# Performance work log

Measured on AMD Instinct MI355X. Metric: run time of the kernel, lower is better.

Reference implementation:

```python
import jax, jax.numpy as jnp
import numpy as np

SEQ, BATCH, H = 512, 1024, 64  # hidden == input == 64 (8x8 grid)


def setup_inputs() -> dict:
    key = jax.random.key(0)
    k_x, k_wih, k_whh, k_bih, k_bhh = jax.random.split(key, 5)
    s = 1.0 / np.sqrt(H)  # PyTorch LSTM init scale U(-1/sqrt(H), 1/sqrt(H))
    x = jax.random.normal(k_x, (SEQ, BATCH, 8, 8), dtype=jnp.float32)
    W_ih = jax.random.uniform(k_wih, (4 * H, H), jnp.float32, -s, s)
    W_hh = jax.random.uniform(k_whh, (4 * H, H), jnp.float32, -s, s)
    b_ih = jax.random.uniform(k_bih, (4 * H,), jnp.float32, -s, s)
    b_hh = jax.random.uniform(k_bhh, (4 * H,), jnp.float32, -s, s)
    return {"x": x, "W_ih": W_ih, "W_hh": W_hh, "b_ih": b_ih, "b_hh": b_hh}


def _lstm(x_flat, W_ih, W_hh, b_ih, b_hh):
    # x_flat: (seq, batch, H). PyTorch gate order: i, f, g, o.
    seq, batch, _ = x_flat.shape
    # Precompute input projections for all timesteps in one big GEMM.
    xg = jnp.einsum('sbh,gh->sbg', x_flat, W_ih) + (b_ih + b_hh)  # (seq, batch, 4H)

    def step(carry, xg_t):
        h, c = carry
        gates = xg_t + h @ W_hh.T  # (batch, 4H)
        i, f, g, o = jnp.split(gates, 4, axis=-1)
        i = jax.nn.sigmoid(i)
        f = jax.nn.sigmoid(f)
        g = jnp.tanh(g)
        o = jax.nn.sigmoid(o)
        c = f * c + i * g
        h = o * jnp.tanh(c)
        return (h, c), h

    h0 = jnp.zeros((batch, W_hh.shape[1]), x_flat.dtype)
    c0 = jnp.zeros_like(h0)
    _, hs = jax.lax.scan(step, (h0, c0), xg)
    return hs  # (seq, batch, H)


def reference(x, W_ih, W_hh, b_ih, b_hh):
    seq, batch = x.shape[0], x.shape[1]
    x_flat = x.reshape(seq, batch, 64)  # Flatten(start_dim=2)
    hs = _lstm(x_flat, W_ih, W_hh, b_ih, b_hh)
    return hs.reshape(-1, 1024, 8, 8)
```

## Files before the change

kernel.cpp:

```cpp
#include <hip/hip_runtime.h>
#include <hip/hip_bf16.h>

#define SEQ   512
#define BATCH 1024
#define HD    64
#define NS    2
#define TB    16

typedef __attribute__((ext_vector_type(8))) short bf16x8;
typedef __attribute__((ext_vector_type(4))) float f32x4;

__device__ __forceinline__ unsigned short f2bf(float f) {
    unsigned u = __float_as_uint(f);
    return (unsigned short)((u + 0x7FFFu + ((u >> 16) & 1u)) >> 16);
}
__device__ __forceinline__ float frcp(float x) { return __builtin_amdgcn_rcpf(x); }
__device__ __forceinline__ float fsig(float x) { return frcp(1.f + __expf(-x)); }
__device__ __forceinline__ float ftanh(float x) { return 1.f - 2.f * frcp(__expf(2.f * x) + 1.f); }

__global__ __launch_bounds__(256, 2)
void lstm_v10(const float* __restrict__ x,
              const float* __restrict__ W_ih,
              const float* __restrict__ W_hh,
              const float* __restrict__ b_ih,
              const float* __restrict__ b_hh,
              float* __restrict__ out)
{
    __shared__ __align__(16) unsigned short xch[TB][NS][72];
    __shared__ __align__(16) float xg[NS][16][16][18];
    __shared__ __align__(16) unsigned short hb[2][NS][80];

    const int tid  = threadIdx.x;
    const int w    = tid >> 6;
    const int ln   = tid & 63;
    const int col  = ln & 15;
    const int kg   = ln >> 4;
    const int slot = (ln >> 2) & 1;
    const int q    = ln >> 4;
    const int qc   = q & 1;
    const int unit = w * 16 + col;
    const int sBase = blockIdx.x * NS;

    bf16x8 Bx[4][2], Bh[4][2];
    #pragma unroll
    for (int g = 0; g < 4; ++g) {
        #pragma unroll
        for (int kt = 0; kt < 2; ++kt) {
            const int n = (g * 4 + w) * 16 + col;
            const int k = kt * 32 + kg * 8;
            const float4 xa = *(const float4*)(W_ih + n * 64 + k);
            const float4 xb = *(const float4*)(W_ih + n * 64 + k + 4);
            const float4 ha = *(const float4*)(W_hh + n * 64 + k);
            const float4 hbq = *(const float4*)(W_hh + n * 64 + k + 4);
            bf16x8 vx, vh;
            vx[0]=(short)f2bf(xa.x); vx[1]=(short)f2bf(xa.y); vx[2]=(short)f2bf(xa.z); vx[3]=(short)f2bf(xa.w);
            vx[4]=(short)f2bf(xb.x); vx[5]=(short)f2bf(xb.y); vx[6]=(short)f2bf(xb.z); vx[7]=(short)f2bf(xb.w);
            vh[0]=(short)f2bf(ha.x); vh[1]=(short)f2bf(ha.y); vh[2]=(short)f2bf(ha.z); vh[3]=(short)f2bf(ha.w);
            vh[4]=(short)f2bf(hbq.x); vh[5]=(short)f2bf(hbq.y); vh[6]=(short)f2bf(hbq.z); vh[7]=(short)f2bf(hbq.w);
            Bx[g][kt] = vx; Bh[g][kt] = vh;
        }
    }
    float bs[4];
    #pragma unroll
    for (int g = 0; g < 4; ++g)
        bs[g] = b_ih[g * 64 + unit] + b_hh[g * 64 + unit];

    if (tid < 160) ((unsigned*)hb)[tid] = 0;

    float c_st = 0.f;
    int p = 0;
    const f32x4 z4 = {0.f, 0.f, 0.f, 0.f};
    float* outp = out + (size_t)(sBase + qc) * HD + unit;

    for (int T = 0; T < SEQ; T += TB) {
        #pragma unroll
        for (int j = 0; j < 2; ++j) {
            const int idx = tid + j * 256;
            const int k4 = idx & 15, sl = (idx >> 4) & 1, tt = idx >> 5;
            const float4 v = *(const float4*)&x[(((size_t)(T + tt) * BATCH) + sBase + sl) * HD + k4 * 4];
            uint2 pk;
            pk.x = (unsigned)f2bf(v.x) | ((unsigned)f2bf(v.y) << 16);
            pk.y = (unsigned)f2bf(v.z) | ((unsigned)f2bf(v.w) << 16);
            *(uint2*)&xch[tt][sl][k4 * 4] = pk;
        }
        __syncthreads();

        #pragma unroll
        for (int m = 0; m < NS; ++m) {
            const bf16x8 a0 = *(const bf16x8*)&xch[ln & 15][m][kg * 8];
            const bf16x8 a1 = *(const bf16x8*)&xch[ln & 15][m][32 + kg * 8];
            #pragma unroll
            for (int g = 0; g < 4; ++g) {
                f32x4 a = __builtin_amdgcn_mfma_f32_16x16x32_bf16(a0, Bx[g][0], z4, 0, 0, 0);
                a = __builtin_amdgcn_mfma_f32_16x16x32_bf16(a1, Bx[g][1], a, 0, 0, 0);
                *(f32x4*)&xg[m][g * 4 + w][col][4 * kg] = a;
            }
        }

        for (int tc = 0; tc < TB; ++tc) {
            const int t = T + tc;
            const float xgi = xg[qc][0 * 4 + w][col][tc];
            const float xgf = xg[qc][1 * 4 + w][col][tc];
            const float xgg = xg[qc][2 * 4 + w][col][tc];
            const float xgo = xg[qc][3 * 4 + w][col][tc];
            const bf16x8 ah0 = *(const bf16x8*)&hb[p][slot][kg * 8];
            const bf16x8 ah1 = *(const bf16x8*)&hb[p][slot][32 + kg * 8];

            __builtin_amdgcn_s_setprio(1);
            f32x4 a0 = __builtin_amdgcn_mfma_f32_16x16x32_bf16(ah0, Bh[0][0], z4, 0, 0, 0);
            f32x4 a1 = __builtin_amdgcn_mfma_f32_16x16x32_bf16(ah0, Bh[1][0], z4, 0, 0, 0);
            f32x4 a2 = __builtin_amdgcn_mfma_f32_16x16x32_bf16(ah0, Bh[2][0], z4, 0, 0, 0);
            f32x4 a3 = __builtin_amdgcn_mfma_f32_16x16x32_bf16(ah0, Bh[3][0], z4, 0, 0, 0);
            a0 = __builtin_amdgcn_mfma_f32_16x16x32_bf16(ah1, Bh[0][1], a0, 0, 0, 0);
            a1 = __builtin_amdgcn_mfma_f32_16x16x32_bf16(ah1, Bh[1][1], a1, 0, 0, 0);
            a2 = __builtin_amdgcn_mfma_f32_16x16x32_bf16(ah1, Bh[2][1], a2, 0, 0, 0);
            a3 = __builtin_amdgcn_mfma_f32_16x16x32_bf16(ah1, Bh[3][1], a3, 0, 0, 0);
            __builtin_amdgcn_s_setprio(0);

            if (ln < 32) {
                const float gi = xgi + a0[0] + bs[0];
                const float gf = xgf + a1[0] + bs[1];
                const float gg = xgg + a2[0] + bs[2];
                const float go = xgo + a3[0] + bs[3];
                const float iv = fsig(gi);
                const float fv = fsig(gf);
                const float gv = ftanh(gg);
                const float ov = fsig(go);
                c_st = fv * c_st + iv * gv;
                const float h  = ov * ftanh(c_st);
                outp[(size_t)t * (BATCH * HD)] = h;
                hb[p ^ 1][q][unit] = f2bf(h);
            }
            p ^= 1;
            __syncthreads();
        }
    }
}

extern "C" void kernel_launch(void* const* d_in, const int* in_sizes, int n_in,
                              void* d_out, int out_size, void* d_ws, size_t ws_size,
                              hipStream_t stream) {
    const float* x    = (const float*)d_in[0];
    const float* W_ih = (const float*)d_in[1];
    const float* W_hh = (const float*)d_in[2];
    const float* b_ih = (const float*)d_in[3];
    const float* b_hh = (const float*)d_in[4];
    float* out = (float*)d_out;

    lstm_v10<<<BATCH / NS, 256, 0, stream>>>(x, W_ih, W_hh, b_ih, b_hh, out);
}
```

Before: 191.1 us.

## Process four sequences per block and fold activation scaling into bf16 weights

Raises batch rows per block from 2 to 4 so all four MFMA row-quads do useful work, which halves the grid to 256 blocks at one block per CU. Pre-scales weights and bias by -log2(e) (or -2·log2(e) for the g gate) so activations become raw v_exp_f32 plus rcp, with tanh rewritten through sigmoid. Bias is folded into the MFMA accumulator init, the xg loads for the next step are issued early, the timestep loop is unrolled, and the MFMAs are split into independent K halves. Risks are lower occupancy with fewer blocks and extra bf16 rounding error from the scaled weights.

```diff
diff --git a/kernel.cpp b/kernel.cpp
--- a/kernel.cpp
+++ b/kernel.cpp
@@ -4,7 +4,7 @@
 #define SEQ   512
 #define BATCH 1024
 #define HD    64
-#define NS    2
+#define NS    4
 #define TB    16
 
 typedef __attribute__((ext_vector_type(8))) short bf16x8;
@@ -15,35 +15,39 @@
     return (unsigned short)((u + 0x7FFFu + ((u >> 16) & 1u)) >> 16);
 }
 __device__ __forceinline__ float frcp(float x) { return __builtin_amdgcn_rcpf(x); }
-__device__ __forceinline__ float fsig(float x) { return frcp(1.f + __expf(-x)); }
-__device__ __forceinline__ float ftanh(float x) { return 1.f - 2.f * frcp(__expf(2.f * x) + 1.f); }
+__device__ __forceinline__ float fexp2(float x) {
+    float r; asm("v_exp_f32 %0, %1" : "=v"(r) : "v"(x)); return r;
+}
 
-__global__ __launch_bounds__(256, 2)
-void lstm_v10(const float* __restrict__ x,
+__global__ __launch_bounds__(256, 1)
+void lstm_v11(const float* __restrict__ x,
               const float* __restrict__ W_ih,
               const float* __restrict__ W_hh,
               const float* __restrict__ b_ih,
               const float* __restrict__ b_hh,
               float* __restrict__ out)
 {
-    __shared__ __align__(16) unsigned short xch[TB][NS][72];
-    __shared__ __align__(16) float xg[NS][16][16][18];
-    __shared__ __align__(16) unsigned short hb[2][NS][80];
+    __shared__ __align__(16) float xg[NS][16][16][20];
+    __shared__ __align__(16) unsigned short xch[NS][TB][72];
+    __shared__ __align__(16) unsigned short hb[2][NS][88];
 
     const int tid  = threadIdx.x;
     const int w    = tid >> 6;
     const int ln   = tid & 63;
     const int col  = ln & 15;
     const int kg   = ln >> 4;
-    const int slot = (ln >> 2) & 1;
+    const int slot = (ln >> 2) & 3;
     const int q    = ln >> 4;
-    const int qc   = q & 1;
     const int unit = w * 16 + col;
     const int sBase = blockIdx.x * NS;
+
+    const float L2E = 1.4426950408889634f;
+    const float sc[4] = { -L2E, -L2E, -2.f * L2E, -L2E };
 
     bf16x8 Bx[4][2], Bh[4][2];
     #pragma unroll
     for (int g = 0; g < 4; ++g) {
+        const float s = sc[g];
         #pragma unroll
         for (int kt = 0; kt < 2; ++kt) {
             const int n = (g * 4 + w) * 16 + col;
@@ -51,87 +55,99 @@
             const float4 xa = *(const float4*)(W_ih + n * 64 + k);
             const float4 xb = *(const float4*)(W_ih + n * 64 + k + 4);
             const float4 ha = *(const float4*)(W_hh + n * 64 + k);
-            const float4 hbq = *(const float4*)(W_hh + n * 64 + k + 4);
+            const float4 hc = *(const float4*)(W_hh + n * 64 + k + 4);
             bf16x8 vx, vh;
-            vx[0]=(short)f2bf(xa.x); vx[1]=(short)f2bf(xa.y); vx[2]=(short)f2bf(xa.z); vx[3]=(short)f2bf(xa.w);
-            vx[4]=(short)f2bf(xb.x); vx[5]=(short)f2bf(xb.y); vx[6]=(short)f2bf(xb.z); vx[7]=(short)f2bf(xb.w);
-            vh[0]=(short)f2bf(ha.x); vh[1]=(short)f2bf(ha.y); vh[2]=(short)f2bf(ha.z); vh[3]=(short)f2bf(ha.w);
-            vh[4]=(short)f2bf(hbq.x); vh[5]=(short)f2bf(hbq.y); vh[6]=(short)f2bf(hbq.z); vh[7]=(short)f2bf(hbq.w);
+            vx[0]=(short)f2bf(xa.x*s); vx[1]=(short)f2bf(xa.y*s); vx[2]=(short)f2bf(xa.z*s); vx[3]=(short)f2bf(xa.w*s);
+            vx[4]=(short)f2bf(xb.x*s); vx[5]=(short)f2bf(xb.y*s); vx[6]=(short)f2bf(xb.z*s); vx[7]=(short)f2bf(xb.w*s);
+            vh[0]=(short)f2bf(ha.x*s); vh[1]=(short)f2bf(ha.y*s); vh[2]=(short)f2bf(ha.z*s); vh[3]=(short)f2bf(ha.w*s);
+            vh[4]=(short)f2bf(hc.x*s); vh[5]=(short)f2bf(hc.y*s); vh[6]=(short)f2bf(hc.z*s); vh[7]=(short)f2bf(hc.w*s);
             Bx[g][kt] = vx; Bh[g][kt] = vh;
         }
     }
-    float bs[4];
+    f32x4 bias4[4];
     #pragma unroll
-    for (int g = 0; g < 4; ++g)
-        bs[g] = b_ih[g * 64 + unit] + b_hh[g * 64 + unit];
+    for (int g = 0; g < 4; ++g) {
+        const int gg = g * 64 + unit;
+        const float b = (b_ih[gg] + b_hh[gg]) * sc[g];
+        bias4[g][0] = b; bias4[g][1] = b; bias4[g][2] = b; bias4[g][3] = b;
+    }
 
-    if (tid < 160) ((unsigned*)hb)[tid] = 0;
+    for (int i = tid; i < (2 * NS * 88) / 2; i += 256) ((unsigned*)hb)[i] = 0;
 
     float c_st = 0.f;
-    int p = 0;
     const f32x4 z4 = {0.f, 0.f, 0.f, 0.f};
-    float* outp = out + (size_t)(sBase + qc) * HD + unit;
+    float* outp = out + (size_t)(sBase + q) * HD + unit;
 
     for (int T = 0; T < SEQ; T += TB) {
         #pragma unroll
-        for (int j = 0; j < 2; ++j) {
+        for (int j = 0; j < 4; ++j) {
             const int idx = tid + j * 256;
-            const int k4 = idx & 15, sl = (idx >> 4) & 1, tt = idx >> 5;
-            const float4 v = *(const float4*)&x[(((size_t)(T + tt) * BATCH) + sBase + sl) * HD + k4 * 4];
+            const int k4 = idx & 15, tt = (idx >> 4) & 15, m = idx >> 8;
+            const float4 v = *(const float4*)&x[(((size_t)(T + tt) * BATCH) + sBase + m) * HD + k4 * 4];
             uint2 pk;
             pk.x = (unsigned)f2bf(v.x) | ((unsigned)f2bf(v.y) << 16);
             pk.y = (unsigned)f2bf(v.z) | ((unsigned)f2bf(v.w) << 16);
-            *(uint2*)&xch[tt][sl][k4 * 4] = pk;
+            *(uint2*)&xch[m][tt][k4 * 4] = pk;
         }
         __syncthreads();
 
         #pragma unroll
         for (int m = 0; m < NS; ++m) {
-            const bf16x8 a0 = *(const bf16x8*)&xch[ln & 15][m][kg * 8];
-            const bf16x8 a1 = *(const bf16x8*)&xch[ln & 15][m][32 + kg * 8];
+            const bf16x8 a0 = *(const bf16x8*)&xch[m][ln & 15][kg * 8];
+            const bf16x8 a1 = *(const bf16x8*)&xch[m][ln & 15][32 + kg * 8];
             #pragma unroll
             for (int g = 0; g < 4; ++g) {
-                f32x4 a = __builtin_amdgcn_mfma_f32_16x16x32_bf16(a0, Bx[g][0], z4, 0, 0, 0);
+                f32x4 a = __builtin_amdgcn_mfma_f32_16x16x32_bf16(a0, Bx[g][0], bias4[g], 0, 0, 0);
                 a = __builtin_amdgcn_mfma_f32_16x16x32_bf16(a1, Bx[g][1], a, 0, 0, 0);
                 *(f32x4*)&xg[m][g * 4 + w][col][4 * kg] = a;
             }
         }
 
+        float xgi = xg[q][0 * 4 + w][col][0];
+        float xgf = xg[q][1 * 4 + w][col][0];
+        float xgg = xg[q][2 * 4 + w][col][0];
+        float xgo = xg[q][3 * 4 + w][col][0];
+
+        #pragma unroll
         for (int tc = 0; tc < TB; ++tc) {
-            const int t = T + tc;
-            const float xgi = xg[qc][0 * 4 + w][col][tc];
-            const float xgf = xg[qc][1 * 4 + w][col][tc];
-            const float xgg = xg[qc][2 * 4 + w][col][tc];
-            const float xgo = xg[qc][3 * 4 + w][col][tc];
-            const bf16x8 ah0 = *(const bf16x8*)&hb[p][slot][kg * 8];
-            const bf16x8 ah1 = *(const bf16x8*)&hb[p][slot][32 + kg * 8];
+            const int pr = tc & 1;
+            const bf16x8 ah0 = *(const bf16x8*)&hb[pr][slot][kg * 8];
+            const bf16x8 ah1 = *(const bf16x8*)&hb[pr][slot][32 + kg * 8];
 
-            __builtin_amdgcn_s_setprio(1);
-            f32x4 a0 = __builtin_amdgcn_mfma_f32_16x16x32_bf16(ah0, Bh[0][0], z4, 0, 0, 0);
-            f32x4 a1 = __builtin_amdgcn_mfma_f32_16x16x32_bf16(ah0, Bh[1][0], z4, 0, 0, 0);
-            f32x4 a2 = __builtin_amdgcn_mfma_f32_16x16x32_bf16(ah0, Bh[2][0], z4, 0, 0, 0);
-            f32x4 a3 = __builtin_amdgcn_mfma_f32_16x16x32_bf16(ah0, Bh[3][0], z4, 0, 0, 0);
-            a0 = __builtin_amdgcn_mfma_f32_16x16x32_bf16(ah1, Bh[0][1], a0, 0, 0, 0);
-            a1 = __builtin_amdgcn_mfma_f32_16x16x32_bf16(ah1, Bh[1][1], a1, 0, 0, 0);
-            a2 = __builtin_amdgcn_mfma_f32_16x16x32_bf16(ah1, Bh[2][1], a2, 0, 0, 0);
-            a3 = __builtin_amdgcn_mfma_f32_16x16x32_bf16(ah1, Bh[3][1], a3, 0, 0, 0);
-            __builtin_amdgcn_s_setprio(0);
+            const f32x4 il = __builtin_amdgcn_mfma_f32_16x16x32_bf16(ah0, Bh[0][0], z4, 0, 0, 0);
+            const f32x4 ih = __builtin_amdgcn_mfma_f32_16x16x32_bf16(ah1, Bh[0][1], z4, 0, 0, 0);
+            const f32x4 fl = __builtin_amdgcn_mfma_f32_16x16x32_bf16(ah0, Bh[1][0], z4, 0, 0, 0);
+            const f32x4 fh = __builtin_amdgcn_mfma_f32_16x16x32_bf16(ah1, Bh[1][1], z4, 0, 0, 0);
+            const f32x4 gl = __builtin_amdgcn_mfma_f32_16x16x32_bf16(ah0, Bh[2][0], z4, 0, 0, 0);
+            const f32x4 gh = __builtin_amdgcn_mfma_f32_16x16x32_bf16(ah1, Bh[2][1], z4, 0, 0, 0);
+            const f32x4 ol = __builtin_amdgcn_mfma_f32_16x16x32_bf16(ah0, Bh[3][0], z4, 0, 0, 0);
+            const f32x4 oh = __builtin_amdgcn_mfma_f32_16x16x32_bf16(ah1, Bh[3][1], z4, 0, 0, 0);
 
-            if (ln < 32) {
-                const float gi = xgi + a0[0] + bs[0];
-                const float gf = xgf + a1[0] + bs[1];
-                const float gg = xgg + a2[0] + bs[2];
-                const float go = xgo + a3[0] + bs[3];
-                const float iv = fsig(gi);
-                const float fv = fsig(gf);
-                const float gv = ftanh(gg);
-                const float ov = fsig(go);
-                c_st = fv * c_st + iv * gv;
-                const float h  = ov * ftanh(c_st);
-                outp[(size_t)t * (BATCH * HD)] = h;
-                hb[p ^ 1][q][unit] = f2bf(h);
+            const float Pi = xgi + il[0] + ih[0];
+            const float Pf = xgf + fl[0] + fh[0];
+            const float Pg = xgg + gl[0] + gh[0];
+            const float Po = xgo + ol[0] + oh[0];
+
+            const float iv = frcp(1.f + fexp2(Pi));
+            const float fv = frcp(1.f + fexp2(Pf));
+            const float gs = frcp(1.f + fexp2(Pg));
+            const float ov = frcp(1.f + fexp2(Po));
+            const float gv = fmaf(2.f, gs, -1.f);
+            c_st = fmaf(fv, c_st, iv * gv);
+            const float tr = frcp(1.f + fexp2(c_st * (-2.f * L2E)));
+            const float h  = fmaf(ov + ov, tr, -ov);
+
+            unsigned hu;
+            asm("v_cvt_pk_bf16_f32 %0, %1, %2" : "=v"(hu) : "v"(h), "v"(0.f));
+            hb[pr ^ 1][q][unit] = (unsigned short)hu;
+
+            outp[(size_t)(T + tc) * (BATCH * HD)] = h;
+            if (tc + 1 < TB) {
+                xgi = xg[q][0 * 4 + w][col][tc + 1];
+                xgf = xg[q][1 * 4 + w][col][tc + 1];
+                xgg = xg[q][2 * 4 + w][col][tc + 1];
+                xgo = xg[q][3 * 4 + w][col][tc + 1];
             }
-            p ^= 1;
             __syncthreads();
         }
     }
@@ -147,5 +163,5 @@
     const float* b_hh = (const float*)d_in[4];
     float* out = (float*)d_out;
 
-    lstm_v10<<<BATCH / NS, 256, 0, stream>>>(x, W_ih, W_hh, b_ih, b_hh, out);
+    lstm_v11<<<BATCH / NS, 256, 0, stream>>>(x, W_ih, W_hh, b_ih, b_hh, out);
 }
```

Result: faster. 161.3 us (-15.6%).
